# Performance work log

Hardware: AMD Instinct MI355X
Metric: run time of the kernel (lower is better)

## Reference

```python
import jax, jax.numpy as jnp
import numpy as np

SCALE = 64 ** (-0.5)  # dim_head**-0.5; heads/dim_head otherwise unused in forward


def setup_inputs() -> dict:
    key = jax.random.key(0)
    ks = jax.random.split(key, 7)
    B, C, T = 8, 512, 4096
    s = C ** (-0.5)  # conv1d default init scale-ish
    x = jax.random.normal(ks[0], (B, C, T), dtype=jnp.float32)
    Wq = jax.random.normal(ks[1], (C, C), dtype=jnp.float32) * s
    bq = jax.random.normal(ks[2], (C,), dtype=jnp.float32) * s
    Wk = jax.random.normal(ks[3], (C, C), dtype=jnp.float32) * s
    bk = jax.random.normal(ks[4], (C,), dtype=jnp.float32) * s
    Wv = jax.random.normal(ks[5], (C, C), dtype=jnp.float32) * s
    bv = jax.random.normal(ks[6], (C,), dtype=jnp.float32) * s
    return {"x": x, "Wq": Wq, "bq": bq, "Wk": Wk, "bk": bk, "Wv": Wv, "bv": bv}


def reference(x, Wq, bq, Wk, bk, Wv, bv):
    # 1x1 Conv1d == per-timestep linear over channels: (o,c) x (b,c,t) -> (b,o,t)
    q = jnp.einsum('oc,bct->bot', Wq, x) + bq[None, :, None]
    k = jnp.einsum('oc,bct->bot', Wk, x) + bk[None, :, None]
    v = jnp.einsum('oc,bct->bot', Wv, x) + bv[None, :, None]
    # Channel-channel attention: dots (b, C, C); softmax over last (channel) axis
    dots = jnp.einsum('bct,bdt->bcd', q, k) * SCALE
    attn = jax.nn.softmax(dots, axis=-1)
    # (b,C,C) x (b,C,t) -> (b,C,t); dropout p=0 and to_out unused in original forward
    out = jnp.einsum('bcd,bdt->bct', attn, v)
    return out
```

## Files before the change

kernel.cpp:

```cpp
#include <hip/hip_runtime.h>

#define B_ 8
#define C_ 512
#define T_ 4096

typedef __attribute__((ext_vector_type(8))) __bf16 bf16x8;
typedef __attribute__((ext_vector_type(8))) _Float16 f16x8;
typedef __attribute__((ext_vector_type(8))) unsigned short u16x8;
typedef __attribute__((ext_vector_type(4))) float f32x4;

__device__ __forceinline__ unsigned short f2bf(float f) {
  unsigned int u = __float_as_uint(f);
  u += 0x7fffu + ((u >> 16) & 1u);
  return (unsigned short)(u >> 16);
}
__device__ __forceinline__ float bf2f(unsigned short h) {
  return __uint_as_float(((unsigned int)h) << 16);
}
__device__ __forceinline__ unsigned short f2h(float f) {
  return __builtin_bit_cast(unsigned short, (_Float16)f);
}

__device__ __forceinline__ void async16(unsigned short* ldsdst, const unsigned short* gsrc) {
  __builtin_amdgcn_global_load_lds(
      (__attribute__((address_space(1))) void*)(void*)const_cast<unsigned short*>(gsrc),
      (__attribute__((address_space(3))) void*)(void*)ldsdst,
      16, 0, 0);
}

template <bool F16>
__device__ __forceinline__ f32x4 mfma16(u16x8 a, u16x8 b, f32x4 c) {
  if constexpr (F16)
    return __builtin_amdgcn_mfma_f32_16x16x32_f16(
        __builtin_bit_cast(f16x8, a), __builtin_bit_cast(f16x8, b), c, 0, 0, 0);
  else
    return __builtin_amdgcn_mfma_f32_16x16x32_bf16(
        __builtin_bit_cast(bf16x8, a), __builtin_bit_cast(bf16x8, b), c, 0, 0, 0);
}

struct GemmP {
  const unsigned short* Ah; const unsigned short* Al; long sA; int lda;
  const unsigned short* Bh; const unsigned short* Bl; long sB; int ldb;
  float* Cf; unsigned short* Ch; unsigned short* Cl; long sC; int ldc;
  int kspan; int zparts;
  const float* rowv; const float* colv; const float* bq; const float* bk;
};

enum { EPI_F32 = 0, EPI_OUT = 1, EPI_DOTS = 2, EPI_SPLIT = 3, EPI_F16 = 4 };

template <int BM, int BN, int WM, int WN, bool SA, bool SB, int EPI, bool F16, int SWZ>
__global__ __launch_bounds__((BM / WM) * (BN / WN) * 64) void gemm_nt(GemmP g) {
  constexpr int KC = 64;
  constexpr int NWAVE = (BM / WM) * (BN / WN);
  constexpr int NT = NWAVE * 64;
  constexpr int ASZ = BM * KC, BSZ = BN * KC;
  constexpr int STAGE = (SA ? 2 : 1) * ASZ + (SB ? 2 : 1) * BSZ;
  constexpr int EPAD = BN + 4;
  constexpr int EPIB = 32 * EPAD * 4;
  constexpr int LDSB = (STAGE * 2 > EPIB) ? STAGE * 2 : EPIB;
  __shared__ alignas(16) char ldsraw[LDSB];
  unsigned short* lds = (unsigned short*)ldsraw;
  unsigned short* ldsAh = lds;
  unsigned short* ldsAl = lds + ASZ;
  unsigned short* ldsBh = lds + (SA ? 2 : 1) * ASZ;
  unsigned short* ldsBl = ldsBh + BSZ;

  const int tid = threadIdx.x;
  const int lane = tid & 63, wid = tid >> 6;
  constexpr int WNB = BN / WN;
  const int wm = wid / WNB, wn = wid % WNB;
  constexpr int MF = WM / 16, NF = WN / 16;

  int bm, bn, z;
  if constexpr (SWZ == 1) {
    const int blk = blockIdx.x;
    const int r = blk & 7, q = blk >> 3;
    const int tri = q % 10, zq = q / 10;
    const int tm = (tri >= 6) ? 3 : (tri >= 3) ? 2 : (tri >= 1) ? 1 : 0;
    bm = tm; bn = tri - (tm * (tm + 1)) / 2;
    z = zq * 8 + r;
  } else if constexpr (SWZ == 2) {
    const int blk = blockIdx.x;
    const int r = blk & 7, q = blk >> 3;
    bm = q & 3;
    const int w = q >> 2;
    bn = ((w & 1) << 3) + r;
    z = w >> 1;
  } else {
    bm = blockIdx.x; bn = blockIdx.y; z = blockIdx.z;
  }
  const int b = z / g.zparts, kp = z - b * g.zparts;

  const unsigned short* Ah = g.Ah + (size_t)b * g.sA + (size_t)kp * g.kspan;
  const unsigned short* Al = SA ? (g.Al + (size_t)b * g.sA + (size_t)kp * g.kspan) : nullptr;
  const unsigned short* Bh = g.Bh + (size_t)b * g.sB + (size_t)kp * g.kspan;
  const unsigned short* Bl = SB ? (g.Bl + (size_t)b * g.sB + (size_t)kp * g.kspan) : nullptr;

  f32x4 acc[MF][NF] = {};

  const int kIters = g.kspan / KC;
  for (int kt = 0; kt < kIters; ++kt) {
    const int kb = kt * KC;
#pragma unroll
    for (int r = 0; r < ASZ / (8 * NT); ++r) {
      int idx = tid + r * NT;
      int row = idx >> 3, sl = idx & 7;
      int kc = (sl ^ (row & 7)) << 3;
      size_t goff = (size_t)(bm * BM + row) * g.lda + kb + kc;
      async16(&ldsAh[idx << 3], Ah + goff);
      if constexpr (SA) async16(&ldsAl[idx << 3], Al + goff);
    }
#pragma unroll
    for (int r = 0; r < BSZ / (8 * NT); ++r) {
      int idx = tid + r * NT;
      int row = idx >> 3, sl = idx & 7;
      int kc = (sl ^ (row & 7)) << 3;
      size_t goff = (size_t)(bn * BN + row) * g.ldb + kb + kc;
      async16(&ldsBh[idx << 3], Bh + goff);
      if constexpr (SB) async16(&ldsBl[idx << 3], Bl + goff);
    }
    __syncthreads();

    const int rsel = lane & 15, kq = lane >> 4;
#pragma unroll
    for (int ks = 0; ks < KC; ks += 32) {
      const int chunk = (ks >> 3) + kq;
      u16x8 afh[MF], afl[MF], bfh[NF], bfl[NF];
#pragma unroll
      for (int fm = 0; fm < MF; ++fm) {
        int row = wm * WM + fm * 16 + rsel;
        int ro = row * KC + ((chunk ^ (row & 7)) << 3);
        afh[fm] = *(const u16x8*)&ldsAh[ro];
        if constexpr (SA) afl[fm] = *(const u16x8*)&ldsAl[ro];
      }
#pragma unroll
      for (int fn = 0; fn < NF; ++fn) {
        int row = wn * WN + fn * 16 + rsel;
        int ro = row * KC + ((chunk ^ (row & 7)) << 3);
        bfh[fn] = *(const u16x8*)&ldsBh[ro];
        if constexpr (SB) bfl[fn] = *(const u16x8*)&ldsBl[ro];
      }
#pragma unroll
      for (int fm = 0; fm < MF; ++fm)
#pragma unroll
        for (int fn = 0; fn < NF; ++fn) {
          acc[fm][fn] = mfma16<F16>(afh[fm], bfh[fn], acc[fm][fn]);
          if constexpr (SB) acc[fm][fn] = mfma16<F16>(afh[fm], bfl[fn], acc[fm][fn]);
          if constexpr (SA) acc[fm][fn] = mfma16<F16>(afl[fm], bfh[fn], acc[fm][fn]);
        }
    }
    __syncthreads();
  }

  if constexpr (EPI == EPI_SPLIT || EPI == EPI_F16) {
#pragma unroll
    for (int fm = 0; fm < MF; ++fm)
#pragma unroll
      for (int fn = 0; fn < NF; ++fn)
#pragma unroll
        for (int r = 0; r < 4; ++r) {
          int i = bm * BM + wm * WM + fm * 16 + ((lane >> 4) << 2) + r;
          int j = bn * BN + wn * WN + fn * 16 + (lane & 15);
          float v = acc[fm][fn][r];
          size_t co = (size_t)z * g.sC + (size_t)i * g.ldc + j;
          if constexpr (EPI == EPI_SPLIT) {
            unsigned short h = f2bf(v);
            g.Ch[co] = h;
            g.Cl[co] = f2bf(v - bf2f(h));
          } else {
            g.Ch[co] = f2h(v);
          }
        }
  } else {
    float* eb = (float*)ldsraw;
#pragma unroll
    for (int ck = 0; ck < BM / 32; ++ck) {
      if (wm == (ck * 32) / WM) {
        const int fm0 = ((ck * 32) % WM) / 16;
#pragma unroll
        for (int fi = 0; fi < 2; ++fi) {
          int fm = fm0 + fi;
#pragma unroll
          for (int fn = 0; fn < NF; ++fn)
#pragma unroll
            for (int r = 0; r < 4; ++r) {
              int lrow = fi * 16 + ((lane >> 4) << 2) + r;
              int col = wn * WN + fn * 16 + (lane & 15);
              eb[lrow * EPAD + col] = acc[fm][fn][r];
            }
        }
      }
      __syncthreads();
#pragma unroll
      for (int it = 0; it < (32 * BN / 4) / NT; ++it) {
        int idx = it * NT + tid;
        int row = idx / (BN / 4), c4 = (idx % (BN / 4)) * 4;
        f32x4 v = *(f32x4*)&eb[row * EPAD + c4];
        int grow = bm * BM + ck * 32 + row;
        int j = bn * BN + c4;
        if constexpr (EPI == EPI_OUT) v = v + g.rowv[b * C_ + grow];
        if constexpr (EPI == EPI_DOTS) {
          f32x4 bkv = *(const f32x4*)&g.bk[j];
          f32x4 ksv = *(const f32x4*)&g.colv[b * C_ + j];
          float qsi = g.rowv[b * C_ + grow], bqi = g.bq[grow];
          v = 0.125f * (v + qsi * bkv + bqi * (ksv + 4096.f * bkv));
        }
        *(f32x4*)&g.Cf[(size_t)z * g.sC + (size_t)grow * g.ldc + j] = v;
      }
      __syncthreads();
    }
  }
}

#define NXB (64 * 8 * 8)
#define PAD 66
__global__ __launch_bounds__(256) void prep_fused(
    const float* __restrict__ x, const float* __restrict__ Wq,
    const float* __restrict__ Wk, const float* __restrict__ Wv,
    unsigned short* __restrict__ Xh, unsigned short* __restrict__ XhT,
    float* __restrict__ S, unsigned short* Wqh, unsigned short* Wql,
    unsigned short* Wkh, unsigned short* Wkl, unsigned short* WvT) {
  __shared__ unsigned short tile[64 * PAD];
  const int tid = threadIdx.x;
  if (blockIdx.x < NXB) {
    const int tl = blockIdx.x;
    const int t0 = (tl & 63) << 6, c0 = ((tl >> 6) & 7) << 6, b = tl >> 9;
    const float* xin = x + ((size_t)(b * C_ + c0)) * T_ + t0;
    unsigned short* xo = Xh + ((size_t)(b * C_ + c0)) * T_ + t0;
#pragma unroll
    for (int r = 0; r < 4; ++r) {
      int p = tid + r * 256;
      int row = p >> 4, c4 = (p & 15) << 2;
      float4 v = *(const float4*)&xin[(size_t)row * T_ + c4];
      unsigned short h0 = f2h(v.x), h1 = f2h(v.y), h2 = f2h(v.z), h3 = f2h(v.w);
      ushort4 hv; hv.x = h0; hv.y = h1; hv.z = h2; hv.w = h3;
      *(ushort4*)&xo[(size_t)row * T_ + c4] = hv;
      unsigned int lo = (unsigned int)h0 | ((unsigned int)h1 << 16);
      unsigned int hi = (unsigned int)h2 | ((unsigned int)h3 << 16);
      ((unsigned int*)&tile[row * PAD + c4])[0] = lo;
      ((unsigned int*)&tile[row * PAD + c4])[1] = hi;
      float s = v.x + v.y + v.z + v.w;
#pragma unroll
      for (int o = 1; o < 16; o <<= 1) s += __shfl_xor(s, o);
      if ((tid & 15) == 0) atomicAdd(&S[b * C_ + c0 + row], s);
    }
    __syncthreads();
#pragma unroll
    for (int r = 0; r < 2; ++r) {
      int idx = tid + r * 256;
      int trow = idx >> 3, cc = (idx & 7) << 3;
      unsigned short vals[8];
#pragma unroll
      for (int j = 0; j < 8; ++j) vals[j] = tile[(cc + j) * PAD + trow];
      *(uint4*)&XhT[((size_t)b * T_ + t0 + trow) * C_ + c0 + cc] = *(uint4*)vals;
    }
  } else {
    int i = (blockIdx.x - NXB) * 256 + tid;
    float q = Wq[i]; unsigned short qh = f2bf(q); Wqh[i] = qh; Wql[i] = f2bf(q - bf2f(qh));
    float k = Wk[i]; unsigned short kh = f2bf(k); Wkh[i] = kh; Wkl[i] = f2bf(k - bf2f(kh));
    float v = Wv[i]; int d = i >> 9, e = i & 511;
    WvT[(e << 9) + d] = f2h(v);
  }
}

__global__ __launch_bounds__(256) void combine_g(const float* __restrict__ gp,
                                                 unsigned short* __restrict__ gh,
                                                 unsigned short* __restrict__ gl) {
  __shared__ float tile[64 * 65];
  const int blk = blockIdx.x;
  const int b = blk & 7, q = blk >> 3;
  const int tr = q >> 3, tc = q & 7;
  const bool mirror = (tr >> 1) < (tc >> 1);
  const int sr = mirror ? tc : tr, sc = mirror ? tr : tc;
  const float* src = gp + ((size_t)b << 21) + (size_t)(sr << 6) * 512 + (sc << 6);
  const int row = threadIdx.x >> 4, c4 = (threadIdx.x & 15) << 2;
  float vals[4][4];
#pragma unroll
  for (int rr = 0; rr < 4; ++rr) {
    const int r = row + rr * 16;
    f32x4 v = {};
#pragma unroll
    for (int p = 0; p < 8; ++p)
      v += *(const f32x4*)&src[((size_t)p << 18) + (size_t)r * 512 + c4];
    if (mirror) {
#pragma unroll
      for (int k = 0; k < 4; ++k) tile[r * 65 + c4 + k] = v[k];
    } else {
#pragma unroll
      for (int k = 0; k < 4; ++k) vals[rr][k] = v[k];
    }
  }
  if (mirror) {
    __syncthreads();
#pragma unroll
    for (int rr = 0; rr < 4; ++rr) {
      const int r = row + rr * 16;
#pragma unroll
      for (int k = 0; k < 4; ++k) vals[rr][k] = tile[(c4 + k) * 65 + r];
    }
  }
  unsigned short* ghp = gh + ((size_t)b << 18) + (size_t)(tr << 6) * 512 + (tc << 6);
  unsigned short* glp = gl + ((size_t)b << 18) + (size_t)(tr << 6) * 512 + (tc << 6);
#pragma unroll
  for (int rr = 0; rr < 4; ++rr) {
    const int r = row + rr * 16;
    ushort4 h, l;
    h.x = f2bf(vals[rr][0]); l.x = f2bf(vals[rr][0] - bf2f(h.x));
    h.y = f2bf(vals[rr][1]); l.y = f2bf(vals[rr][1] - bf2f(h.y));
    h.z = f2bf(vals[rr][2]); l.z = f2bf(vals[rr][2] - bf2f(h.z));
    h.w = f2bf(vals[rr][3]); l.w = f2bf(vals[rr][3] - bf2f(h.w));
    *(ushort4*)&ghp[(size_t)r * 512 + c4] = h;
    *(ushort4*)&glp[(size_t)r * 512 + c4] = l;
  }
}

__global__ __launch_bounds__(256) void qs_ks(const float* __restrict__ Wq, const float* __restrict__ Wk,
                                             const float* __restrict__ s, float* __restrict__ qs,
                                             float* __restrict__ ks) {
  int lane = threadIdx.x & 63, wid = threadIdx.x >> 6;
  int gi = blockIdx.x * 4 + wid;
  int b = gi >> 9, i = gi & 511;
  const float* sv = s + (b << 9);
  const float* wqr = Wq + (size_t)i * C_;
  const float* wkr = Wk + (size_t)i * C_;
  float aq = 0.f, ak = 0.f;
#pragma unroll
  for (int c = lane; c < C_; c += 64) {
    float sc = sv[c];
    aq += wqr[c] * sc;
    ak += wkr[c] * sc;
  }
#pragma unroll
  for (int o = 32; o > 0; o >>= 1) { aq += __shfl_down(aq, o); ak += __shfl_down(ak, o); }
  if (lane == 0) { qs[gi] = aq; ks[gi] = ak; }
}

__global__ __launch_bounds__(256) void softmax_rows(const float* __restrict__ logits,
                                                    const float* __restrict__ bv,
                                                    unsigned short* __restrict__ attn,
                                                    float* __restrict__ ab) {
  const int row = blockIdx.x;
  const int tid = threadIdx.x, lane = tid & 63, wid = tid >> 6;
  const float* L = logits + (size_t)row * C_;
  float v0 = L[tid], v1 = L[tid + 256];
  __shared__ float red[4];
  float m = fmaxf(v0, v1);
#pragma unroll
  for (int o = 32; o > 0; o >>= 1) m = fmaxf(m, __shfl_down(m, o));
  if (lane == 0) red[wid] = m;
  __syncthreads();
  m = fmaxf(fmaxf(red[0], red[1]), fmaxf(red[2], red[3]));
  __syncthreads();
  float e0 = __expf(v0 - m), e1 = __expf(v1 - m);
  float sum = e0 + e1;
#pragma unroll
  for (int o = 32; o > 0; o >>= 1) sum += __shfl_down(sum, o);
  if (lane == 0) red[wid] = sum;
  __syncthreads();
  sum = red[0] + red[1] + red[2] + red[3];
  float inv = 1.f / sum;
  float a0 = e0 * inv, a1 = e1 * inv;
  unsigned short* ar = attn + (size_t)row * C_;
  ar[tid] = f2h(a0);
  ar[tid + 256] = f2h(a1);
  float abv = a0 * bv[tid] + a1 * bv[tid + 256];
  __syncthreads();
#pragma unroll
  for (int o = 32; o > 0; o >>= 1) abv += __shfl_down(abv, o);
  if (lane == 0) red[wid] = abv;
  __syncthreads();
  if (tid == 0) ab[row] = red[0] + red[1] + red[2] + red[3];
}

extern "C" void kernel_launch(void* const* d_in, const int* in_sizes, int n_in,
                              void* d_out, int out_size, void* d_ws, size_t ws_size,
                              hipStream_t stream) {
  const float* x  = (const float*)d_in[0];
  const float* Wq = (const float*)d_in[1];
  const float* bq = (const float*)d_in[2];
  const float* Wk = (const float*)d_in[3];
  const float* bk = (const float*)d_in[4];
  const float* Wv = (const float*)d_in[5];
  const float* bv = (const float*)d_in[6];
  float* out = (float*)d_out;

  char* ws = (char*)d_ws;
  size_t off = 0;
  auto alloc = [&](size_t bytes) {
    char* p = ws + off;
    off += (bytes + 255) & ~(size_t)255;
    return p;
  };
  const size_t XSZ = (size_t)B_ * C_ * T_;
  const size_t GSZ = (size_t)B_ * C_ * C_;

  unsigned short* Xh  = (unsigned short*)alloc(XSZ * 2);
  unsigned short* XhT = (unsigned short*)alloc(XSZ * 2);
  float* Gpart = (float*)alloc((size_t)8 * GSZ * 4);
  unsigned short* Gh = (unsigned short*)alloc(GSZ * 2);
  unsigned short* Gl = (unsigned short*)alloc(GSZ * 2);
  unsigned short* Ph = (unsigned short*)alloc(GSZ * 2);
  unsigned short* Pl = (unsigned short*)alloc(GSZ * 2);
  float* Logits = (float*)alloc(GSZ * 4);
  unsigned short* Attn = (unsigned short*)alloc(GSZ * 2);
  unsigned short* Mh = (unsigned short*)alloc(GSZ * 2);
  unsigned short* Wqh = (unsigned short*)alloc((size_t)C_ * C_ * 2);
  unsigned short* Wql = (unsigned short*)alloc((size_t)C_ * C_ * 2);
  unsigned short* Wkh = (unsigned short*)alloc((size_t)C_ * C_ * 2);
  unsigned short* Wkl = (unsigned short*)alloc((size_t)C_ * C_ * 2);
  unsigned short* WvT = (unsigned short*)alloc((size_t)C_ * C_ * 2);
  float* S  = (float*)alloc((size_t)B_ * C_ * 4);
  float* Qs = (float*)alloc((size_t)B_ * C_ * 4);
  float* Ks = (float*)alloc((size_t)B_ * C_ * 4);
  float* Ab = (float*)alloc((size_t)B_ * C_ * 4);

  hipMemsetAsync(S, 0, (size_t)B_ * C_ * 4, stream);
  prep_fused<<<NXB + C_ * C_ / 256, 256, 0, stream>>>(x, Wq, Wk, Wv, Xh, XhT, S,
                                                      Wqh, Wql, Wkh, Wkl, WvT);
  qs_ks<<<B_ * C_ / 4, 256, 0, stream>>>(Wq, Wk, S, Qs, Ks);

  {
    GemmP p = {};
    p.Ah = Xh; p.sA = (long)C_ * T_; p.lda = T_;
    p.Bh = Xh; p.sB = (long)C_ * T_; p.ldb = T_;
    p.Cf = Gpart; p.sC = (long)C_ * C_; p.ldc = C_;
    p.kspan = T_ / 8; p.zparts = 8;
    gemm_nt<128, 128, 32, 64, false, false, EPI_F32, true, 1>
        <<<640, 512, 0, stream>>>(p);
  }
  combine_g<<<B_ * 64, 256, 0, stream>>>(Gpart, Gh, Gl);

  {
    GemmP p = {};
    p.Ah = Wqh; p.Al = Wql; p.sA = 0; p.lda = C_;
    p.Bh = Gh; p.Bl = Gl; p.sB = (long)C_ * C_; p.ldb = C_;
    p.Ch = Ph; p.Cl = Pl; p.sC = (long)C_ * C_; p.ldc = C_;
    p.kspan = C_; p.zparts = 1;
    gemm_nt<64, 64, 32, 32, true, true, EPI_SPLIT, false, 0>
        <<<dim3(8, 8, 8), 256, 0, stream>>>(p);
  }
  {
    GemmP p = {};
    p.Ah = Ph; p.Al = Pl; p.sA = (long)C_ * C_; p.lda = C_;
    p.Bh = Wkh; p.Bl = Wkl; p.sB = 0; p.ldb = C_;
    p.Cf = Logits; p.sC = (long)C_ * C_; p.ldc = C_;
    p.kspan = C_; p.zparts = 1;
    p.rowv = Qs; p.colv = Ks; p.bq = bq; p.bk = bk;
    gemm_nt<64, 64, 32, 32, true, true, EPI_DOTS, false, 0>
        <<<dim3(8, 8, 8), 256, 0, stream>>>(p);
  }
  softmax_rows<<<B_ * C_, 256, 0, stream>>>(Logits, bv, Attn, Ab);
  {
    GemmP p = {};
    p.Ah = Attn; p.sA = (long)C_ * C_; p.lda = C_;
    p.Bh = WvT; p.sB = 0; p.ldb = C_;
    p.Ch = Mh; p.sC = (long)C_ * C_; p.ldc = C_;
    p.kspan = C_; p.zparts = 1;
    gemm_nt<64, 64, 32, 32, false, false, EPI_F16, true, 0>
        <<<dim3(8, 8, 8), 256, 0, stream>>>(p);
  }
  {
    GemmP p = {};
    p.Ah = Mh; p.sA = (long)C_ * C_; p.lda = C_;
    p.Bh = XhT; p.sB = (long)C_ * T_; p.ldb = C_;
    p.Cf = out; p.sC = (long)C_ * T_; p.ldc = T_;
    p.kspan = C_; p.zparts = 1;
    p.rowv = Ab;
    gemm_nt<128, 256, 64, 64, false, false, EPI_OUT, true, 2>
        <<<512, 512, 0, stream>>>(p);
  }
  (void)in_sizes; (void)n_in; (void)out_size; (void)ws_size;
}
```

Before: 234.0 us.

## Restructure x conversion blocks, move row sums to separate kernel, add nontemporal hints

Each prep block now covers 64 channels by 256 timesteps in four stages, prefetching the next 64-column slab while it transposes the current one. The per-row atomicAdd sums and the memset are replaced by a separate sum_rows kernel that reduces the fp16 Xh rows. The row sums therefore come from fp16-rounded values rather than fp32, which slightly changes precision. Nontemporal stores and loads are added for the split-K partial G buffer so it does not pollute the cache.

```diff
diff --git a/kernel.cpp b/kernel.cpp
--- a/kernel.cpp
+++ b/kernel.cpp
@@ -205,62 +205,93 @@
           float qsi = g.rowv[b * C_ + grow], bqi = g.bq[grow];
           v = 0.125f * (v + qsi * bkv + bqi * (ksv + 4096.f * bkv));
         }
-        *(f32x4*)&g.Cf[(size_t)z * g.sC + (size_t)grow * g.ldc + j] = v;
+        __builtin_nontemporal_store(
+            v, (f32x4*)&g.Cf[(size_t)z * g.sC + (size_t)grow * g.ldc + j]);
       }
       __syncthreads();
     }
   }
 }
 
-#define NXB (64 * 8 * 8)
+#define NXB2 1024
 #define PAD 66
 __global__ __launch_bounds__(256) void prep_fused(
     const float* __restrict__ x, const float* __restrict__ Wq,
     const float* __restrict__ Wk, const float* __restrict__ Wv,
     unsigned short* __restrict__ Xh, unsigned short* __restrict__ XhT,
-    float* __restrict__ S, unsigned short* Wqh, unsigned short* Wql,
+    unsigned short* Wqh, unsigned short* Wql,
     unsigned short* Wkh, unsigned short* Wkl, unsigned short* WvT) {
   __shared__ unsigned short tile[64 * PAD];
   const int tid = threadIdx.x;
-  if (blockIdx.x < NXB) {
+  if (blockIdx.x < NXB2) {
     const int tl = blockIdx.x;
-    const int t0 = (tl & 63) << 6, c0 = ((tl >> 6) & 7) << 6, b = tl >> 9;
+    const int tb = tl & 15, c0 = ((tl >> 4) & 7) << 6, b = tl >> 7;
+    const int t0 = tb << 8;
     const float* xin = x + ((size_t)(b * C_ + c0)) * T_ + t0;
     unsigned short* xo = Xh + ((size_t)(b * C_ + c0)) * T_ + t0;
-#pragma unroll
-    for (int r = 0; r < 4; ++r) {
-      int p = tid + r * 256;
-      int row = p >> 4, c4 = (p & 15) << 2;
-      float4 v = *(const float4*)&xin[(size_t)row * T_ + c4];
-      unsigned short h0 = f2h(v.x), h1 = f2h(v.y), h2 = f2h(v.z), h3 = f2h(v.w);
-      ushort4 hv; hv.x = h0; hv.y = h1; hv.z = h2; hv.w = h3;
-      *(ushort4*)&xo[(size_t)row * T_ + c4] = hv;
-      unsigned int lo = (unsigned int)h0 | ((unsigned int)h1 << 16);
-      unsigned int hi = (unsigned int)h2 | ((unsigned int)h3 << 16);
-      ((unsigned int*)&tile[row * PAD + c4])[0] = lo;
-      ((unsigned int*)&tile[row * PAD + c4])[1] = hi;
-      float s = v.x + v.y + v.z + v.w;
-#pragma unroll
-      for (int o = 1; o < 16; o <<= 1) s += __shfl_xor(s, o);
-      if ((tid & 15) == 0) atomicAdd(&S[b * C_ + c0 + row], s);
-    }
-    __syncthreads();
-#pragma unroll
-    for (int r = 0; r < 2; ++r) {
-      int idx = tid + r * 256;
-      int trow = idx >> 3, cc = (idx & 7) << 3;
-      unsigned short vals[8];
-#pragma unroll
-      for (int j = 0; j < 8; ++j) vals[j] = tile[(cc + j) * PAD + trow];
-      *(uint4*)&XhT[((size_t)b * T_ + t0 + trow) * C_ + c0 + cc] = *(uint4*)vals;
+    const int row16 = tid >> 4, c4 = (tid & 15) << 2;
+    float4 v[4];
+#pragma unroll
+    for (int r = 0; r < 4; ++r)
+      v[r] = *(const float4*)&xin[(size_t)(row16 + r * 16) * T_ + c4];
+    for (int st = 0; st < 4; ++st) {
+      if (st) __syncthreads();
+#pragma unroll
+      for (int r = 0; r < 4; ++r) {
+        int row = row16 + r * 16;
+        unsigned short h0 = f2h(v[r].x), h1 = f2h(v[r].y),
+                       h2 = f2h(v[r].z), h3 = f2h(v[r].w);
+        ushort4 hv; hv.x = h0; hv.y = h1; hv.z = h2; hv.w = h3;
+        *(ushort4*)&xo[(size_t)row * T_ + st * 64 + c4] = hv;
+        unsigned int lo = (unsigned int)h0 | ((unsigned int)h1 << 16);
+        unsigned int hi = (unsigned int)h2 | ((unsigned int)h3 << 16);
+        ((unsigned int*)&tile[row * PAD + c4])[0] = lo;
+        ((unsigned int*)&tile[row * PAD + c4])[1] = hi;
+      }
+      float4 nv[4];
+      if (st < 3) {
+#pragma unroll
+        for (int r = 0; r < 4; ++r)
+          nv[r] = *(const float4*)&xin[(size_t)(row16 + r * 16) * T_ + (st + 1) * 64 + c4];
+      }
+      __syncthreads();
+#pragma unroll
+      for (int r = 0; r < 2; ++r) {
+        int idx = tid + r * 256;
+        int trow = idx >> 3, cc = (idx & 7) << 3;
+        unsigned short vals[8];
+#pragma unroll
+        for (int j = 0; j < 8; ++j) vals[j] = tile[(cc + j) * PAD + trow];
+        *(uint4*)&XhT[((size_t)b * T_ + t0 + st * 64 + trow) * C_ + c0 + cc] =
+            *(uint4*)vals;
+      }
+#pragma unroll
+      for (int r = 0; r < 4; ++r) v[r] = nv[r];
     }
   } else {
-    int i = (blockIdx.x - NXB) * 256 + tid;
+    int i = (blockIdx.x - NXB2) * 256 + tid;
     float q = Wq[i]; unsigned short qh = f2bf(q); Wqh[i] = qh; Wql[i] = f2bf(q - bf2f(qh));
     float k = Wk[i]; unsigned short kh = f2bf(k); Wkh[i] = kh; Wkl[i] = f2bf(k - bf2f(kh));
     float v = Wv[i]; int d = i >> 9, e = i & 511;
     WvT[(e << 9) + d] = f2h(v);
   }
+}
+
+__global__ __launch_bounds__(256) void sum_rows(const unsigned short* __restrict__ xh,
+                                                float* __restrict__ S) {
+  const int row = blockIdx.x * 4 + (threadIdx.x >> 6);
+  const int lane = threadIdx.x & 63;
+  const unsigned short* r = xh + (size_t)row * T_;
+  float s = 0.f;
+#pragma unroll
+  for (int i = 0; i < 8; ++i) {
+    f16x8 v = *(const f16x8*)&r[(i * 64 + lane) * 8];
+#pragma unroll
+    for (int j = 0; j < 8; ++j) s += (float)v[j];
+  }
+#pragma unroll
+  for (int o = 32; o > 0; o >>= 1) s += __shfl_down(s, o);
+  if (lane == 0) S[row] = s;
 }
 
 __global__ __launch_bounds__(256) void combine_g(const float* __restrict__ gp,
@@ -281,7 +312,8 @@
     f32x4 v = {};
 #pragma unroll
     for (int p = 0; p < 8; ++p)
-      v += *(const f32x4*)&src[((size_t)p << 18) + (size_t)r * 512 + c4];
+      v += __builtin_nontemporal_load(
+          (const f32x4*)&src[((size_t)p << 18) + (size_t)r * 512 + c4]);
     if (mirror) {
 #pragma unroll
       for (int k = 0; k < 4; ++k) tile[r * 65 + c4 + k] = v[k];
@@ -414,9 +446,9 @@
   float* Ks = (float*)alloc((size_t)B_ * C_ * 4);
   float* Ab = (float*)alloc((size_t)B_ * C_ * 4);
 
-  hipMemsetAsync(S, 0, (size_t)B_ * C_ * 4, stream);
-  prep_fused<<<NXB + C_ * C_ / 256, 256, 0, stream>>>(x, Wq, Wk, Wv, Xh, XhT, S,
-                                                      Wqh, Wql, Wkh, Wkl, WvT);
+  prep_fused<<<NXB2 + C_ * C_ / 256, 256, 0, stream>>>(x, Wq, Wk, Wv, Xh, XhT,
+                                                       Wqh, Wql, Wkh, Wkl, WvT);
+  sum_rows<<<B_ * C_ / 4, 256, 0, stream>>>(Xh, S);
   qs_ks<<<B_ * C_ / 4, 256, 0, stream>>>(Wq, Wk, S, Qs, Ks);
 
   {
```

New measurement: 231.3 us. Within noise of the previous version (-1.1%).
